# Kernel optimization log

Hardware: AMD Instinct MI355X
Metric: run time of the kernel (lower is better)

The kernel has to match this reference:

```python
import jax, jax.numpy as jnp
import numpy as np

TOL = 5
SEG_PENALTY = 2.0
SEG_REWARD = 1.0
PROX_REWARD = 2.0
FAR_PENALTY = 1.5
CLASS_WEIGHTS = np.array([0.1, 0.1, 5.0, 5.0], dtype=np.float32)


def setup_inputs() -> dict:
    key = jax.random.key(0)
    k1, k2, k3 = jax.random.split(key, 3)
    B, S, C = 128, 32768, 4
    logits = jax.random.normal(k1, (B, S, C), dtype=jnp.float32)
    labels = jax.random.randint(k2, (B, S), 0, 4, dtype=jnp.int32)
    seg_marks = jax.random.randint(k3, (B, S), 0, 2, dtype=jnp.int32)
    return {"logits": logits, "labels": labels, "seg_marks": seg_marks}


def _window_any(x_bool, tol):
    # sliding 'any' over a symmetric window of size 2*tol+1 along the seq axis
    xi = x_bool.astype(jnp.int32)
    w = jax.lax.reduce_window(xi, 0, jax.lax.max, (1, 2 * tol + 1), (1, 1), 'SAME')
    return w > 0


def reference(logits, labels, seg_marks):
    B, S, C = logits.shape
    weights = jnp.asarray(CLASS_WEIGHTS)

    # weighted cross-entropy, reduction='none', ignore_index=-100
    ignored = labels == -100
    safe_labels = jnp.where(ignored, 0, labels)
    logz = jax.nn.logsumexp(logits, axis=-1)                       # [B,S]
    picked = jnp.take_along_axis(logits, safe_labels[..., None], axis=-1)[..., 0]
    base_loss = weights[safe_labels] * (logz - picked)
    base_loss = jnp.where(ignored, 0.0, base_loss)

    predictions = jnp.argmax(logits, axis=-1)
    pred_sw = predictions >= 2                                      # [B,S]
    true_sw = labels >= 2                                           # [B,S]

    adj = jnp.zeros_like(base_loss)

    # segmentation alignment: gated by pred_sw
    seg_pos = seg_marks > 0
    zcol = jnp.zeros((B, 1), dtype=bool)
    seg_prev1 = jnp.concatenate([zcol, seg_pos[:, :-1]], axis=1)    # seg[t-1]>0
    seg_prev2 = jnp.concatenate([zcol, zcol, seg_pos[:, :-2]], axis=1)
    seg_next1 = jnp.concatenate([seg_pos[:, 1:], zcol], axis=1)     # seg[t+1]>0
    penalty_cond = seg_prev1 | seg_prev2                            # break => add once
    reward_cond = seg_pos | seg_next1                               # if/elif => once
    adj = adj + pred_sw * (SEG_PENALTY * penalty_cond.astype(jnp.float32)
                           - SEG_REWARD * reward_cond.astype(jnp.float32))

    # proximity reward: true switch with any predicted switch within +/- TOL
    pred_near = _window_any(pred_sw, TOL)
    adj = adj - PROX_REWARD * (true_sw & pred_near).astype(jnp.float32)

    # far penalty: predicted switch with no true switch within +/- TOL
    # (only applies when the row has at least one true switch)
    true_near = _window_any(true_sw, TOL)
    has_true = jnp.any(true_sw, axis=1, keepdims=True)
    adj = adj + FAR_PENALTY * (pred_sw & has_true & (~true_near)).astype(jnp.float32)

    adjusted = base_loss + adj
    valid = (labels != -100).astype(jnp.float32)
    return (adjusted * valid).sum() / valid.sum()
```

## Files before the change

kernel.cpp:

```cpp
#include <hip/hip_runtime.h>


typedef unsigned long long u64;
typedef __attribute__((ext_vector_type(4))) float f32x4;

#define PPT 4
#define POSW (64 * PPT)
#define NT 256
#define WPB (NT / 64)
#define GRID 4096
#define NPARTS (GRID * WPB)

#if __has_builtin(__builtin_amdgcn_exp2f)
#define EXP2F(x) __builtin_amdgcn_exp2f(x)
#else
#define EXP2F(x) exp2f(x)
#endif
#if __has_builtin(__builtin_amdgcn_logf)
#define LOG2F(x) __builtin_amdgcn_logf(x)
#else
#define LOG2F(x) log2f(x)
#endif

static __global__ __launch_bounds__(NT) void
loss_kernel(const float4* __restrict__ logits, const int* __restrict__ labels,
            const int* __restrict__ seg, float* __restrict__ parts) {
    const int S = 32768;
    const int t = threadIdx.x;
    const int w = t >> 6, lane = t & 63;
    const int gw = blockIdx.x * WPB + w;
    const int b = gw >> 7;
    const int span = (gw & 127) * POSW;

    const size_t rowoff = (size_t)b * S;
    const float4* lrow = logits + rowoff;
    const int* labrow = labels + rowoff;
    const int* segrow = seg + rowoff;

    const int p0 = span + lane;
    float4 g[PPT];
    int lab[PPT], sg[PPT];
#pragma unroll
    for (int j = 0; j < PPT; ++j) g[j] = lrow[p0 + j * 64];
#pragma unroll
    for (int j = 0; j < PPT; ++j) lab[j] = labrow[p0 + j * 64];
#pragma unroll
    for (int j = 0; j < PPT; ++j) sg[j] = segrow[p0 + j * 64];

    const bool fl = lane < 5;
    const bool use = (lane < 10) && (fl ? (span > 0) : (span + POSW < S));
    const int fpos = fl ? (span - 5 + lane) : (span + POSW + lane - 5);
    float4 fg = make_float4(0.f, 0.f, 0.f, 0.f);
    int flb = 0, fsg = 0;
    if (use) { fg = lrow[fpos]; flb = labrow[fpos]; fsg = segrow[fpos]; }

    asm volatile(""
                 :
                 : "v"(*(const f32x4*)&g[0]), "v"(*(const f32x4*)&g[1]),
                   "v"(*(const f32x4*)&g[2]), "v"(*(const f32x4*)&g[3]),
                   "v"(lab[0]), "v"(lab[1]), "v"(lab[2]), "v"(lab[3]),
                   "v"(sg[0]), "v"(sg[1]), "v"(sg[2]), "v"(sg[3]),
                   "v"(*(const f32x4*)&fg), "v"(flb), "v"(fsg));

    const u64 fbp = __ballot(use && (fmaxf(fg.z, fg.w) > fmaxf(fg.x, fg.y)));
    const u64 fbt = __ballot(use && (flb >= 2));
    const u64 fbs = __ballot(use && (fsg > 0));
    const u64 l5p = fbp & 31u, r5p = (fbp >> 5) & 31u;
    const u64 l5t = fbt & 31u, r5t = (fbt >> 5) & 31u;
    const u64 l5s = fbs & 31u, r5s = (fbs >> 5) & 31u;

    const float L2E = 1.4426950408889634f;
    u64 pm[PPT], tm[PPT], sm[PPT];
    float lg_hi = 0.0f, lg_lo = 0.0f;
    float pk_hi = 0.0f, pk_lo = 0.0f;
#pragma unroll
    for (int j = 0; j < PPT; ++j) {
        const float4 gj = g[j];
        const float mab = fmaxf(gj.x, gj.y), mcd = fmaxf(gj.z, gj.w);
        pm[j] = __ballot(mcd > mab);
        tm[j] = __ballot(lab[j] >= 2);
        sm[j] = __ballot(sg[j] > 0);
        const float se = EXP2F(gj.x * L2E) + EXP2F(gj.y * L2E) +
                         EXP2F(gj.z * L2E) + EXP2F(gj.w * L2E);
        const float l2 = LOG2F(se);
        const float p01 = (lab[j] == 0) ? gj.x : gj.y;
        const float p23 = (lab[j] == 2) ? gj.z : gj.w;
        const float picked = (lab[j] < 2) ? p01 : p23;
        const bool hi = lab[j] >= 2;
        lg_hi += hi ? l2 : 0.0f;
        lg_lo += hi ? 0.0f : l2;
        pk_hi += hi ? picked : 0.0f;
        pk_lo += hi ? 0.0f : picked;
    }

    const unsigned sh_hi = (unsigned)((lane - 10) & 63);
    const bool lo_sel = lane < 32;
    int npen = 0, nrew = 0, nprox = 0, nfar = 0;
#pragma unroll
    for (int j = 0; j < PPT; ++j) {
        const u64 pp5 = j ? (pm[j - 1] >> 59) : l5p;
        const u64 pn5 = (j < PPT - 1) ? (pm[j + 1] & 31u) : r5p;
        const u64 tp5 = j ? (tm[j - 1] >> 59) : l5t;
        const u64 tn5 = (j < PPT - 1) ? (tm[j + 1] & 31u) : r5t;
        const u64 sp5 = j ? (sm[j - 1] >> 59) : l5s;
        const u64 sn5 = (j < PPT - 1) ? (sm[j + 1] & 31u) : r5s;

        const u64 plo = (pm[j] << 5) | pp5;
        const u64 pvh = (plo >> 10) | (((pm[j] >> 59) | (pn5 << 5)) << 54);
        const u64 tlo = (tm[j] << 5) | tp5;
        const u64 tvh = (tlo >> 10) | (((tm[j] >> 59) | (tn5 << 5)) << 54);
        const u64 slo = (sm[j] << 5) | sp5;
        const u64 svh = (slo >> 10) | (((sm[j] >> 59) | (sn5 << 5)) << 54);

        const unsigned wp = (unsigned)(lo_sel ? (plo >> lane) : (pvh >> sh_hi)) & 0x7FFu;
        const unsigned wt = (unsigned)(lo_sel ? (tlo >> lane) : (tvh >> sh_hi)) & 0x7FFu;
        const unsigned ws_ = (unsigned)(lo_sel ? (slo >> lane) : (svh >> sh_hi)) & 0x7FFu;

        const int pred = (wp >> 5) & 1;
        const int tru = (wt >> 5) & 1;
        nprox += (wp != 0u) ? tru : 0;
        nfar += (wt == 0u) ? pred : 0;
        npen += ((ws_ >> 3) & 3u) ? pred : 0;
        nrew += ((ws_ >> 5) & 3u) ? pred : 0;
    }

    const float LN2 = 0.69314718055994531f;
    float tot = 5.0f * (LN2 * lg_hi - pk_hi) + 0.1f * (LN2 * lg_lo - pk_lo) +
                2.0f * (float)npen - (float)nrew - 2.0f * (float)nprox +
                1.5f * (float)nfar;
#pragma unroll
    for (int off = 32; off > 0; off >>= 1) tot += __shfl_down(tot, off);
    if (lane == 0) parts[gw] = tot;
}

static __global__ __launch_bounds__(1024) void
finalize_kernel(const float4* __restrict__ parts4, float* __restrict__ out) {
    const int t = threadIdx.x;
    __shared__ double s_ds[16];
    double ds = 0.0;
#pragma unroll
    for (int k = 0; k < NPARTS / 4096; ++k) {
        const float4 p = parts4[t + k * 1024];
        ds += (double)p.x + (double)p.y + (double)p.z + (double)p.w;
    }
#pragma unroll
    for (int off = 32; off > 0; off >>= 1) ds += __shfl_down(ds, off);
    if ((t & 63) == 0) s_ds[t >> 6] = ds;
    __syncthreads();
    if (t == 0) {
        double Ssum = 0.0;
#pragma unroll
        for (int i = 0; i < 16; ++i) Ssum += s_ds[i];
        out[0] = (float)(Ssum / 4194304.0);
    }
}

extern "C" void kernel_launch(void* const* d_in, const int* in_sizes, int n_in,
                              void* d_out, int out_size, void* d_ws, size_t ws_size,
                              hipStream_t stream) {
    const float4* logits = (const float4*)d_in[0];
    const int* labels = (const int*)d_in[1];
    const int* seg = (const int*)d_in[2];
    float* out = (float*)d_out;

    float* parts = (float*)d_ws;

    loss_kernel<<<GRID, NT, 0, stream>>>(logits, labels, seg, parts);
    finalize_kernel<<<1, 1024, 0, stream>>>((const float4*)parts, out);
}
```

Before: 24.56 us.

## Assign contiguous positions per lane and build windows via lane shuffles

Each lane now handles four consecutive sequence positions instead of positions strided by 64, so labels and seg marks load as one 16-byte vector and logits load contiguously. The sliding-window bitmasks are built by packing per-lane 4-bit flags and exchanging them with neighbouring lanes through four shuffles, replacing the per-element 64-bit ballots and wide shift logic. This cuts load instructions and scalar/64-bit bit manipulation, at the cost of cross-lane shuffles and edge-case patching for the wavefront boundaries.

Measured after the change: 24.39 us. No clear change (-0.7%).

```diff
diff --git a/kernel.cpp b/kernel.cpp
--- a/kernel.cpp
+++ b/kernel.cpp
@@ -37,15 +37,12 @@
     const int* labrow = labels + rowoff;
     const int* segrow = seg + rowoff;
 
-    const int p0 = span + lane;
+    const int q0 = span + 4 * lane;
     float4 g[PPT];
-    int lab[PPT], sg[PPT];
 #pragma unroll
-    for (int j = 0; j < PPT; ++j) g[j] = lrow[p0 + j * 64];
-#pragma unroll
-    for (int j = 0; j < PPT; ++j) lab[j] = labrow[p0 + j * 64];
-#pragma unroll
-    for (int j = 0; j < PPT; ++j) sg[j] = segrow[p0 + j * 64];
+    for (int j = 0; j < PPT; ++j) g[j] = lrow[q0 + j];
+    const int4 la = *(const int4*)(labrow + q0);
+    const int4 sgv = *(const int4*)(segrow + q0);
 
     const bool fl = lane < 5;
     const bool use = (lane < 10) && (fl ? (span > 0) : (span + POSW < S));
@@ -58,64 +55,73 @@
                  :
                  : "v"(*(const f32x4*)&g[0]), "v"(*(const f32x4*)&g[1]),
                    "v"(*(const f32x4*)&g[2]), "v"(*(const f32x4*)&g[3]),
-                   "v"(lab[0]), "v"(lab[1]), "v"(lab[2]), "v"(lab[3]),
-                   "v"(sg[0]), "v"(sg[1]), "v"(sg[2]), "v"(sg[3]),
+                   "v"(la.x), "v"(la.y), "v"(la.z), "v"(la.w),
+                   "v"(sgv.x), "v"(sgv.y), "v"(sgv.z), "v"(sgv.w),
                    "v"(*(const f32x4*)&fg), "v"(flb), "v"(fsg));
 
     const u64 fbp = __ballot(use && (fmaxf(fg.z, fg.w) > fmaxf(fg.x, fg.y)));
     const u64 fbt = __ballot(use && (flb >= 2));
     const u64 fbs = __ballot(use && (fsg > 0));
-    const u64 l5p = fbp & 31u, r5p = (fbp >> 5) & 31u;
-    const u64 l5t = fbt & 31u, r5t = (fbt >> 5) & 31u;
-    const u64 l5s = fbs & 31u, r5s = (fbs >> 5) & 31u;
+    const unsigned l5p = (unsigned)(fbp & 31u), r5p = (unsigned)((fbp >> 5) & 31u);
+    const unsigned l5t = (unsigned)(fbt & 31u), r5t = (unsigned)((fbt >> 5) & 31u);
+    const unsigned l5s = (unsigned)(fbs & 31u), r5s = (unsigned)((fbs >> 5) & 31u);
 
     const float L2E = 1.4426950408889634f;
-    u64 pm[PPT], tm[PPT], sm[PPT];
-    float lg_hi = 0.0f, lg_lo = 0.0f;
-    float pk_hi = 0.0f, pk_lo = 0.0f;
+    const int le[4] = {la.x, la.y, la.z, la.w};
+    const int se_[4] = {sgv.x, sgv.y, sgv.z, sgv.w};
+    unsigned pb = 0, tb = 0, sb = 0;
+    float lg_hi = 0.0f, lg_lo = 0.0f, pk_hi = 0.0f, pk_lo = 0.0f;
 #pragma unroll
-    for (int j = 0; j < PPT; ++j) {
-        const float4 gj = g[j];
+    for (int e = 0; e < PPT; ++e) {
+        const float4 gj = g[e];
         const float mab = fmaxf(gj.x, gj.y), mcd = fmaxf(gj.z, gj.w);
-        pm[j] = __ballot(mcd > mab);
-        tm[j] = __ballot(lab[j] >= 2);
-        sm[j] = __ballot(sg[j] > 0);
-        const float se = EXP2F(gj.x * L2E) + EXP2F(gj.y * L2E) +
-                         EXP2F(gj.z * L2E) + EXP2F(gj.w * L2E);
-        const float l2 = LOG2F(se);
-        const float p01 = (lab[j] == 0) ? gj.x : gj.y;
-        const float p23 = (lab[j] == 2) ? gj.z : gj.w;
-        const float picked = (lab[j] < 2) ? p01 : p23;
-        const bool hi = lab[j] >= 2;
+        pb |= (unsigned)(mcd > mab) << e;
+        tb |= (unsigned)(le[e] >= 2) << e;
+        sb |= (unsigned)(se_[e] > 0) << e;
+        const float sexp = EXP2F(gj.x * L2E) + EXP2F(gj.y * L2E) +
+                           EXP2F(gj.z * L2E) + EXP2F(gj.w * L2E);
+        const float l2 = LOG2F(sexp);
+        const float p01 = (le[e] == 0) ? gj.x : gj.y;
+        const float p23 = (le[e] == 2) ? gj.z : gj.w;
+        const float picked = (le[e] < 2) ? p01 : p23;
+        const bool hi = le[e] >= 2;
         lg_hi += hi ? l2 : 0.0f;
         lg_lo += hi ? 0.0f : l2;
         pk_hi += hi ? picked : 0.0f;
         pk_lo += hi ? 0.0f : picked;
     }
 
-    const unsigned sh_hi = (unsigned)((lane - 10) & 63);
-    const bool lo_sel = lane < 32;
+    const unsigned v = pb | (tb << 4) | (sb << 8);
+    const unsigned um2 = __shfl(v, (lane + 62) & 63);
+    const unsigned um1 = __shfl(v, (lane + 63) & 63);
+    const unsigned up1 = __shfl(v, (lane + 1) & 63);
+    const unsigned up2 = __shfl(v, (lane + 2) & 63);
+
+    const bool e0 = (lane == 0), e1 = (lane == 1);
+    const bool e62 = (lane == 62), e63 = (lane == 63);
+#define ASM20(sh, L5, R5)                                                      \
+    ({                                                                         \
+        unsigned a = ((um2 >> (sh)) & 15u) | (((um1 >> (sh)) & 15u) << 4) |    \
+                     (((v >> (sh)) & 15u) << 8) |                              \
+                     (((up1 >> (sh)) & 15u) << 12) |                           \
+                     (((up2 >> (sh)) & 15u) << 16);                            \
+        a = e0 ? ((a & ~0xFFu) | ((L5) << 3)) : a;                             \
+        a = e1 ? ((a & ~0x8u) | ((((L5) >> 4) & 1u) << 3)) : a;                \
+        a = e62 ? ((a & ~(1u << 16)) | (((R5) & 1u) << 16)) : a;               \
+        a = e63 ? ((a & ~(0x1Fu << 12)) | ((R5) << 12)) : a;                   \
+        a;                                                                     \
+    })
+    const unsigned aP = ASM20(0, l5p, r5p);
+    const unsigned aT = ASM20(4, l5t, r5t);
+    const unsigned aS = ASM20(8, l5s, r5s);
+#undef ASM20
+
     int npen = 0, nrew = 0, nprox = 0, nfar = 0;
 #pragma unroll
-    for (int j = 0; j < PPT; ++j) {
-        const u64 pp5 = j ? (pm[j - 1] >> 59) : l5p;
-        const u64 pn5 = (j < PPT - 1) ? (pm[j + 1] & 31u) : r5p;
-        const u64 tp5 = j ? (tm[j - 1] >> 59) : l5t;
-        const u64 tn5 = (j < PPT - 1) ? (tm[j + 1] & 31u) : r5t;
-        const u64 sp5 = j ? (sm[j - 1] >> 59) : l5s;
-        const u64 sn5 = (j < PPT - 1) ? (sm[j + 1] & 31u) : r5s;
-
-        const u64 plo = (pm[j] << 5) | pp5;
-        const u64 pvh = (plo >> 10) | (((pm[j] >> 59) | (pn5 << 5)) << 54);
-        const u64 tlo = (tm[j] << 5) | tp5;
-        const u64 tvh = (tlo >> 10) | (((tm[j] >> 59) | (tn5 << 5)) << 54);
-        const u64 slo = (sm[j] << 5) | sp5;
-        const u64 svh = (slo >> 10) | (((sm[j] >> 59) | (sn5 << 5)) << 54);
-
-        const unsigned wp = (unsigned)(lo_sel ? (plo >> lane) : (pvh >> sh_hi)) & 0x7FFu;
-        const unsigned wt = (unsigned)(lo_sel ? (tlo >> lane) : (tvh >> sh_hi)) & 0x7FFu;
-        const unsigned ws_ = (unsigned)(lo_sel ? (slo >> lane) : (svh >> sh_hi)) & 0x7FFu;
-
+    for (int e = 0; e < PPT; ++e) {
+        const unsigned wp = (aP >> (3 + e)) & 0x7FFu;
+        const unsigned wt = (aT >> (3 + e)) & 0x7FFu;
+        const unsigned ws_ = (aS >> (3 + e)) & 0x7FFu;
         const int pred = (wp >> 5) & 1;
         const int tru = (wt >> 5) & 1;
         nprox += (wp != 0u) ? tru : 0;
```
